# Optimization experiments

Hardware: AMD Instinct MI355X
Metric: run time of the kernel (lower is better)

## Reference

```python
import jax, jax.numpy as jnp
import numpy as np

N, D, F, E, TOP_K = 8192, 1024, 2048, 8, 2


def setup_inputs() -> dict:
    key = jax.random.key(0)
    ks = jax.random.split(key, 8)
    s = 0.02
    x = jax.random.normal(ks[0], (N, D), dtype=jnp.float32)
    Wr = jax.random.normal(ks[1], (D, E), dtype=jnp.float32) * s  # router
    br = jnp.zeros((E,), jnp.float32)
    W1 = jax.random.normal(ks[2], (E, D, F), dtype=jnp.float32) * s  # expert FFN in
    b1 = jnp.zeros((E, F), jnp.float32)
    W2 = jax.random.normal(ks[3], (E, F, D), dtype=jnp.float32) * s  # expert FFN out
    b2 = jnp.zeros((E, D), jnp. float32)
    return {"x": x, "Wr": Wr, "br": br, "W1": W1, "b1": b1, "W2": W2, "b2": b2}


def reference(x, Wr, br, W1, b1, W2, b2):
    # Router: per-token expert logits -> softmax probabilities -> top-k sampler.
    logits = x @ Wr + br                         # [N, E]
    probs = jax.nn.softmax(logits, axis=-1)      # [N, E]
    top_p, top_i = jax.lax.top_k(probs, TOP_K)   # [N, K]
    # Combine weights: prob mass only on the selected top-k experts per token.
    w = (jax.nn.one_hot(top_i, E, dtype=x.dtype) * top_p[..., None]).sum(axis=1)  # [N, E]
    # Per-expert gather-compute-scatter, expressed as masked full-batch expert FFN
    # (identical math: tokens not routed to expert e have weight 0).
    out = jnp.zeros((x.shape[0], W2.shape[-1]), dtype=x.dtype)
    for e in range(E):  # small fixed loop over structurally distinct experts
        h = jax.nn.gelu(x @ W1[e] + b1[e])       # [N, F]
        y = h @ W2[e] + b2[e]                    # [N, D]
        out = out + w[:, e:e + 1] * y            # weighted scatter-add combine
    return out
```

## Files before the change

kernel.cpp:

```cpp
#include <hip/hip_runtime.h>
#include <hip/hip_bf16.h>


#define N_TOK 8192
#define DIM   1024
#define FF    2048
#define NE    8

typedef unsigned short ushort_t;
typedef __bf16 bf16x8 __attribute__((ext_vector_type(8)));
typedef float  f32x4  __attribute__((ext_vector_type(4)));
typedef unsigned short u16x8 __attribute__((ext_vector_type(8)));

__device__ __forceinline__ ushort_t f2bf(float f) {
    union { float f; unsigned int u; } v; v.f = f;
    unsigned int r = (v.u + 0x7FFFu + ((v.u >> 16) & 1u)) >> 16;
    return (ushort_t)r;
}

__device__ __forceinline__ unsigned int pkbf2(float lo, float hi) {
    __hip_bfloat162 h = __float22bfloat162_rn(make_float2(lo, hi));
    return *reinterpret_cast<unsigned int*>(&h);
}

__device__ __forceinline__ void gload_lds16(const ushort_t* g, ushort_t* l) {
    __builtin_amdgcn_global_load_lds(
        (const __attribute__((address_space(1))) void*)g,
        (__attribute__((address_space(3))) void*)l,
        16, 0, 0);
}

__global__ __launch_bounds__(256) void convert_x_kernel(
    const float* __restrict__ x, ushort_t* __restrict__ xb)
{
    size_t i = ((size_t)blockIdx.x * 256 + threadIdx.x) * 8;
    float4 a = *reinterpret_cast<const float4*>(x + i);
    float4 b = *reinterpret_cast<const float4*>(x + i + 4);
    uint4 o;
    o.x = pkbf2(a.x, a.y); o.y = pkbf2(a.z, a.w);
    o.z = pkbf2(b.x, b.y); o.w = pkbf2(b.z, b.w);
    *reinterpret_cast<uint4*>(xb + i) = o;
}

__global__ __launch_bounds__(256) void transpose_conv_kernel(
    const float* __restrict__ in, ushort_t* __restrict__ out, int R, int C)
{
    __shared__ float tile[64][68];
    const int e = blockIdx.z;
    const float* I = in + (size_t)e * R * C;
    ushort_t*    O = out + (size_t)e * R * C;
    const int c0 = blockIdx.x * 64, r0 = blockIdx.y * 64;
    const int tid = threadIdx.x;
#pragma unroll
    for (int j = 0; j < 4; ++j) {
        int row = j * 16 + (tid >> 4);
        int col = (tid & 15) * 4;
        float4 v = *reinterpret_cast<const float4*>(&I[(size_t)(r0 + row) * C + c0 + col]);
        *reinterpret_cast<float4*>(&tile[row][col]) = v;
    }
    __syncthreads();
#pragma unroll
    for (int j = 0; j < 2; ++j) {
        int orow = j * 32 + (tid >> 3);
        int k0   = (tid & 7) * 8;
        uint4 o;
        o.x = pkbf2(tile[k0 + 0][orow], tile[k0 + 1][orow]);
        o.y = pkbf2(tile[k0 + 2][orow], tile[k0 + 3][orow]);
        o.z = pkbf2(tile[k0 + 4][orow], tile[k0 + 5][orow]);
        o.w = pkbf2(tile[k0 + 6][orow], tile[k0 + 7][orow]);
        *reinterpret_cast<uint4*>(&O[(size_t)(c0 + orow) * R + r0 + k0]) = o;
    }
}

__global__ __launch_bounds__(256) void router_kernel(
    const float* __restrict__ x, const float* __restrict__ Wr, const float* __restrict__ br,
    int* __restrict__ cnt, int* __restrict__ tok_list, float* __restrict__ w_list)
{
    __shared__ int   se0[64], se1[64];
    __shared__ float sw0[64], sw1[64];

    const int wid  = threadIdx.x >> 6;
    const int lane = threadIdx.x & 63;
    const int tblk = blockIdx.x * 64;

    for (int i = 0; i < 16; ++i) {
        const int li = wid * 16 + i;
        const int t  = tblk + li;
        const float* xr = x + (size_t)t * DIM;

        float acc[NE];
#pragma unroll
        for (int e = 0; e < NE; ++e) acc[e] = 0.f;
        for (int d = lane; d < DIM; d += 64) {
            float xv = xr[d];
            const float4* w4 = reinterpret_cast<const float4*>(Wr + (size_t)d * NE);
            float4 w0 = w4[0], w1 = w4[1];
            acc[0] += xv * w0.x; acc[1] += xv * w0.y; acc[2] += xv * w0.z; acc[3] += xv * w0.w;
            acc[4] += xv * w1.x; acc[5] += xv * w1.y; acc[6] += xv * w1.z; acc[7] += xv * w1.w;
        }
#pragma unroll
        for (int e = 0; e < NE; ++e) {
            for (int off = 32; off > 0; off >>= 1)
                acc[e] += __shfl_down(acc[e], off, 64);
        }
        if (lane == 0) {
            float l[NE];
#pragma unroll
            for (int e = 0; e < NE; ++e) l[e] = acc[e] + br[e];
            float mx = l[0];
#pragma unroll
            for (int e = 1; e < NE; ++e) mx = fmaxf(mx, l[e]);
            float p[NE], s = 0.f;
#pragma unroll
            for (int e = 0; e < NE; ++e) { p[e] = expf(l[e] - mx); s += p[e]; }
            float inv = 1.f / s;
            int e0 = 0;
#pragma unroll
            for (int e = 1; e < NE; ++e) if (l[e] > l[e0]) e0 = e;
            int e1 = (e0 == 0) ? 1 : 0;
#pragma unroll
            for (int e = 0; e < NE; ++e) if (e != e0 && l[e] > l[e1]) e1 = e;
            se0[li] = e0; sw0[li] = p[e0] * inv;
            se1[li] = e1; sw1[li] = p[e1] * inv;
        }
    }
    __syncthreads();

    if (threadIdx.x < 64) {
        const int t  = tblk + lane;
        const int e0 = se0[lane], e1 = se1[lane];
        const unsigned long long below = ((unsigned long long)1 << lane) - 1;
        int p0 = 0, p1 = 0;
#pragma unroll
        for (int e = 0; e < NE; ++e) {
            unsigned long long m0 = __ballot(e0 == e);
            unsigned long long m1 = __ballot(e1 == e);
            int c = __popcll(m0) + __popcll(m1);
            int b = 0;
            if (lane == e && c) b = atomicAdd(&cnt[e], c);
            b = __shfl(b, e, 64);
            if (e0 == e) p0 = b + __popcll(m0 & below);
            if (e1 == e) p1 = b + __popcll(m0) + __popcll(m1 & below);
        }
        tok_list[e0 * N_TOK + p0] = t;  w_list[e0 * N_TOK + p0] = sw0[lane];
        tok_list[e1 * N_TOK + p1] = t;  w_list[e1 * N_TOK + p1] = sw1[lane];
    }
}

__global__ void scan_kernel(const int* __restrict__ cnt, int* __restrict__ offs,
                            int* __restrict__ tile_e, int* __restrict__ tile_m0,
                            int* __restrict__ meta)
{
    if (threadIdx.x == 0 && blockIdx.x == 0) {
        int s = 0;
        for (int e = 0; e < NE; ++e) { offs[e] = s; s += cnt[e]; }
        offs[NE] = s;
        int nt = 0;
        for (int e = 0; e < NE; ++e)
            for (int m0 = 0; m0 < cnt[e]; m0 += 128) {
                tile_e[nt] = e; tile_m0[nt] = m0; ++nt;
            }
        meta[0] = nt;
    }
}

template <int MODE>
__global__ __launch_bounds__(512, 6) void moe_gemm_kernel(
    const ushort_t* __restrict__ A,
    const ushort_t* __restrict__ Bt,
    const float*    __restrict__ bias,
    const int*      __restrict__ cnt,
    const int*      __restrict__ offs,
    const int*      __restrict__ tok_list,
    const float*    __restrict__ w_list,
    const int*      __restrict__ tile_e,
    const int*      __restrict__ tile_m0,
    const int*      __restrict__ meta,
    ushort_t*       __restrict__ hout,
    float*          __restrict__ out)
{
    const int K    = (MODE == 0) ? 1024 : 2048;
    const int NCOL = (MODE == 0) ? 2048 : 1024;

    const int nmt = meta[0];
    const int L   = nmt << 4;

    const int xcd = blockIdx.x & 7;
    const int q = L >> 3, r = L & 7;
    const int cstart = (xcd < r) ? xcd * (q + 1) : r * (q + 1) + (xcd - r) * q;
    const int clen   = (xcd < r) ? q + 1 : q;

    __shared__ ushort_t smem[24576];
#define ASB(b) (smem + (b) * 4096)
#define BSB(b) (smem + 12288 + (b) * 4096)

    const int tid  = threadIdx.x;
    const int lane = tid & 63;
    const int wid  = tid >> 6;
    const int wr = (wid >> 2) * 64;
    const int wc = (wid & 3) * 32;
    const int la = lane & 15;
    const int kc = lane >> 4;

    for (int i = blockIdx.x >> 3; i < clen; i += 96) {
        const int tau = cstart + i;
        const int mt  = tau >> 4;
        int nb, kh;
        if (MODE == 0) { nb = tau & 15; kh = 0; }
        else           { kh = tau & 1;  nb = (tau >> 1) & 7; }
        const int e   = tile_e[mt];
        const int m0  = tile_m0[mt];
        const int cnt_e  = cnt[e];
        const int offs_e = offs[e];
        const int n0  = nb * 128;
        const int koff = kh << 10;

        __syncthreads();

        const int srow  = tid >> 2;
        const int chunk = (tid & 3) ^ ((srow >> 1) & 3);
        size_t asrc, bsrc;
        {
            int entry = m0 + srow;
            if (MODE == 0) {
                int tok = (entry < cnt_e) ? tok_list[e * N_TOK + entry] : 0;
                asrc = (size_t)tok * K + chunk * 8;
            } else {
                asrc = (size_t)(offs_e + entry) * K + koff + chunk * 8;
            }
            bsrc = ((size_t)e * NCOL + n0 + srow) * K + koff + chunk * 8;
        }

        f32x4 acc[4][2];
#pragma unroll
        for (int m = 0; m < 4; ++m)
#pragma unroll
            for (int n = 0; n < 2; ++n)
                acc[m][n] = (f32x4){0.f, 0.f, 0.f, 0.f};

        auto STAGE = [&](int t, int b) {
            int k0 = t * 32;
            gload_lds16(A  + asrc + k0, ASB(b) + tid * 8);
            gload_lds16(Bt + bsrc + k0, BSB(b) + tid * 8);
        };

        auto COMPUTE = [&](int b) {
            bf16x8 af[4], bfr[2];
#pragma unroll
            for (int m = 0; m < 4; ++m) {
                int rr = wr + m * 16 + la;
                af[m] = *reinterpret_cast<const bf16x8*>(ASB(b) + (rr * 4 + (kc ^ ((rr >> 1) & 3))) * 8);
            }
#pragma unroll
            for (int n = 0; n < 2; ++n) {
                int rr = wc + n * 16 + la;
                bfr[n] = *reinterpret_cast<const bf16x8*>(BSB(b) + (rr * 4 + (kc ^ ((rr >> 1) & 3))) * 8);
            }
            __builtin_amdgcn_s_setprio(1);
#pragma unroll
            for (int m = 0; m < 4; ++m)
#pragma unroll
                for (int n = 0; n < 2; ++n)
                    acc[m][n] = __builtin_amdgcn_mfma_f32_16x16x32_bf16(af[m], bfr[n], acc[m][n], 0, 0, 0);
            __builtin_amdgcn_s_setprio(0);
        };

        const int nk = 32;
        STAGE(0, 0);
        STAGE(1, 1);
        for (int t = 0; t < nk - 1; ++t) {
            asm volatile("s_waitcnt vmcnt(2)" ::: "memory");
            __builtin_amdgcn_s_barrier();
            if (t + 2 < nk) STAGE(t + 2, (t + 2) % 3);
            COMPUTE(t % 3);
        }
        asm volatile("s_waitcnt vmcnt(0)" ::: "memory");
        __builtin_amdgcn_s_barrier();
        COMPUTE((nk - 1) % 3);

        if (MODE == 0) {
            __syncthreads();
#pragma unroll
            for (int m = 0; m < 4; ++m) {
                int rbase = wr + m * 16 + (lane >> 4) * 4;
#pragma unroll
                for (int n = 0; n < 2; ++n) {
                    int ccol = wc + n * 16 + la;
                    float bi = bias[(size_t)e * NCOL + n0 + ccol];
#pragma unroll
                    for (int jj = 0; jj < 4; ++jj) {
                        float v = acc[m][n][jj] + bi;
                        float u = 0.7978845608028654f * (v + 0.044715f * v * v * v);
                        float t2 = __builtin_amdgcn_exp2f(2.8853900817779268f * u);
                        float g = v * (t2 / (t2 + 1.f));
                        smem[(rbase + jj) * 128 + ccol] = f2bf(g);
                    }
                }
            }
            __syncthreads();
#pragma unroll
            for (int j = 0; j < 4; ++j) {
                int c = tid + 512 * j;
                int row  = c >> 4;
                int col8 = (c & 15) * 8;
                int entry = m0 + row;
                if (entry < cnt_e) {
                    u16x8 v = *reinterpret_cast<const u16x8*>(&smem[row * 128 + col8]);
                    *reinterpret_cast<u16x8*>(&hout[(size_t)(offs_e + entry) * FF + n0 + col8]) = v;
                }
            }
        } else {
#pragma unroll
            for (int m = 0; m < 4; ++m) {
                int rbase = wr + m * 16 + (lane >> 4) * 4;
#pragma unroll
                for (int n = 0; n < 2; ++n) {
                    int gcol = n0 + wc + n * 16 + la;
                    float bi = (kh != 0) ? 0.f : bias[(size_t)e * NCOL + gcol];
#pragma unroll
                    for (int jj = 0; jj < 4; ++jj) {
                        int entry = m0 + rbase + jj;
                        if (entry < cnt_e) {
                            float v = acc[m][n][jj] + bi;
                            int tok  = tok_list[e * N_TOK + entry];
                            float w  = w_list  [e * N_TOK + entry];
                            atomicAdd(&out[(size_t)tok * DIM + gcol], w * v);
                        }
                    }
                }
            }
        }
    }
#undef ASB
#undef BSB
}

extern "C" void kernel_launch(void* const* d_in, const int* in_sizes, int n_in,
                              void* d_out, int out_size, void* d_ws, size_t ws_size,
                              hipStream_t stream)
{
    const float* x  = (const float*)d_in[0];
    const float* Wr = (const float*)d_in[1];
    const float* br = (const float*)d_in[2];
    const float* W1 = (const float*)d_in[3];
    const float* b1 = (const float*)d_in[4];
    const float* W2 = (const float*)d_in[5];
    const float* b2 = (const float*)d_in[6];
    float* out = (float*)d_out;

    char* ws = (char*)d_ws;
    size_t off = 0;
    auto alloc = [&](size_t bytes) -> void* {
        void* p = ws + off;
        off = (off + bytes + 255) & ~(size_t)255;
        return p;
    };
    ushort_t* w1t = (ushort_t*)alloc((size_t)NE * DIM * FF * 2);
    ushort_t* w2t = (ushort_t*)alloc((size_t)NE * DIM * FF * 2);
    ushort_t* xb  = (ushort_t*)alloc((size_t)N_TOK * DIM * 2);
    ushort_t* h   = (ushort_t*)alloc(((size_t)2 * N_TOK + 128) * FF * 2);
    int*      cnt = (int*)alloc(NE * sizeof(int));
    int*      offs= (int*)alloc((NE + 1) * sizeof(int));
    int*   tok_list = (int*)alloc((size_t)NE * N_TOK * sizeof(int));
    float* w_list   = (float*)alloc((size_t)NE * N_TOK * sizeof(float));
    int*   tile_e   = (int*)alloc(256 * sizeof(int));
    int*   tile_m0  = (int*)alloc(256 * sizeof(int));
    int*   meta     = (int*)alloc(16 * sizeof(int));
    (void)ws_size; (void)in_sizes; (void)n_in;

    hipMemsetAsync(out, 0, (size_t)out_size * sizeof(float), stream);
    hipMemsetAsync(cnt, 0, NE * sizeof(int), stream);

    convert_x_kernel<<<(N_TOK * DIM) / (8 * 256), 256, 0, stream>>>(x, xb);
    transpose_conv_kernel<<<dim3(FF / 64, DIM / 64, NE), 256, 0, stream>>>(W1, w1t, DIM, FF);
    transpose_conv_kernel<<<dim3(DIM / 64, FF / 64, NE), 256, 0, stream>>>(W2, w2t, FF, DIM);
    router_kernel<<<N_TOK / 64, 256, 0, stream>>>(x, Wr, br, cnt, tok_list, w_list);
    scan_kernel<<<1, 64, 0, stream>>>(cnt, offs, tile_e, tile_m0, meta);

    moe_gemm_kernel<0><<<768, 512, 0, stream>>>(
        xb, w1t, b1, cnt, offs, tok_list, w_list, tile_e, tile_m0, meta, h, nullptr);
    moe_gemm_kernel<1><<<768, 512, 0, stream>>>(
        h, w2t, b2, cnt, offs, tok_list, w_list, tile_e, tile_m0, meta, nullptr, out);
}
```

Baseline: 454.8 us.

## Pre-pack operands into MFMA fragment layout and load directly from global memory

Weights and the gathered token activations are now rearranged into a 16-row by 8-element fragment-packed bf16 layout, so each lane can read its MFMA operand with one 16-byte global load. The LDS staging pipeline and its barriers are removed in favour of register double-buffered direct loads. A new gather kernel builds an expert-sorted, padded activation buffer, which removes the per-tile token indirection in the first GEMM. Occupancy and grid size are lowered from 6 to 4 blocks per CU and from 768 to 512 blocks, and the GEMMs now rely on L2/cache hit rates instead of LDS reuse across waves.

```diff
diff --git a/kernel.cpp b/kernel.cpp
--- a/kernel.cpp
+++ b/kernel.cpp
@@ -6,6 +6,8 @@
 #define DIM   1024
 #define FF    2048
 #define NE    8
+#define ROWS_PAD 16512
+#define MAXTILE  1031
 
 typedef unsigned short ushort_t;
 typedef __bf16 bf16x8 __attribute__((ext_vector_type(8)));
@@ -21,55 +23,6 @@
 __device__ __forceinline__ unsigned int pkbf2(float lo, float hi) {
     __hip_bfloat162 h = __float22bfloat162_rn(make_float2(lo, hi));
     return *reinterpret_cast<unsigned int*>(&h);
-}
-
-__device__ __forceinline__ void gload_lds16(const ushort_t* g, ushort_t* l) {
-    __builtin_amdgcn_global_load_lds(
-        (const __attribute__((address_space(1))) void*)g,
-        (__attribute__((address_space(3))) void*)l,
-        16, 0, 0);
-}
-
-__global__ __launch_bounds__(256) void convert_x_kernel(
-    const float* __restrict__ x, ushort_t* __restrict__ xb)
-{
-    size_t i = ((size_t)blockIdx.x * 256 + threadIdx.x) * 8;
-    float4 a = *reinterpret_cast<const float4*>(x + i);
-    float4 b = *reinterpret_cast<const float4*>(x + i + 4);
-    uint4 o;
-    o.x = pkbf2(a.x, a.y); o.y = pkbf2(a.z, a.w);
-    o.z = pkbf2(b.x, b.y); o.w = pkbf2(b.z, b.w);
-    *reinterpret_cast<uint4*>(xb + i) = o;
-}
-
-__global__ __launch_bounds__(256) void transpose_conv_kernel(
-    const float* __restrict__ in, ushort_t* __restrict__ out, int R, int C)
-{
-    __shared__ float tile[64][68];
-    const int e = blockIdx.z;
-    const float* I = in + (size_t)e * R * C;
-    ushort_t*    O = out + (size_t)e * R * C;
-    const int c0 = blockIdx.x * 64, r0 = blockIdx.y * 64;
-    const int tid = threadIdx.x;
-#pragma unroll
-    for (int j = 0; j < 4; ++j) {
-        int row = j * 16 + (tid >> 4);
-        int col = (tid & 15) * 4;
-        float4 v = *reinterpret_cast<const float4*>(&I[(size_t)(r0 + row) * C + c0 + col]);
-        *reinterpret_cast<float4*>(&tile[row][col]) = v;
-    }
-    __syncthreads();
-#pragma unroll
-    for (int j = 0; j < 2; ++j) {
-        int orow = j * 32 + (tid >> 3);
-        int k0   = (tid & 7) * 8;
-        uint4 o;
-        o.x = pkbf2(tile[k0 + 0][orow], tile[k0 + 1][orow]);
-        o.y = pkbf2(tile[k0 + 2][orow], tile[k0 + 3][orow]);
-        o.z = pkbf2(tile[k0 + 4][orow], tile[k0 + 5][orow]);
-        o.w = pkbf2(tile[k0 + 6][orow], tile[k0 + 7][orow]);
-        *reinterpret_cast<uint4*>(&O[(size_t)(c0 + orow) * R + r0 + k0]) = o;
-    }
 }
 
 __global__ __launch_bounds__(256) void router_kernel(
@@ -147,14 +100,14 @@
     }
 }
 
-__global__ void scan_kernel(const int* __restrict__ cnt, int* __restrict__ offs,
+__global__ void scan_kernel(const int* __restrict__ cnt, int* __restrict__ aoffs,
                             int* __restrict__ tile_e, int* __restrict__ tile_m0,
                             int* __restrict__ meta)
 {
     if (threadIdx.x == 0 && blockIdx.x == 0) {
         int s = 0;
-        for (int e = 0; e < NE; ++e) { offs[e] = s; s += cnt[e]; }
-        offs[NE] = s;
+        for (int e = 0; e < NE; ++e) { aoffs[e] = s; s += (cnt[e] + 15) & ~15; }
+        aoffs[NE] = s;
         int nt = 0;
         for (int e = 0; e < NE; ++e)
             for (int m0 = 0; m0 < cnt[e]; m0 += 128) {
@@ -164,13 +117,74 @@
     }
 }
 
+__global__ __launch_bounds__(256) void gather_pack_kernel(
+    const float* __restrict__ x, const int* __restrict__ cnt,
+    const int* __restrict__ aoffs, const int* __restrict__ tok_list,
+    ushort_t* __restrict__ xpack)
+{
+    const int c   = blockIdx.x * 256 + threadIdx.x;
+    const int row = c >> 7;
+    const int d0  = (c & 127) << 3;
+    int e = 0;
+#pragma unroll
+    for (int k = 1; k < NE; ++k) e += (row >= aoffs[k]);
+    int entry = row - aoffs[e];
+    int ce = cnt[e];
+    if (entry >= ce) entry = (ce > 0) ? ce - 1 : 0;
+    const int tok = tok_list[e * N_TOK + entry] & (N_TOK - 1);
+    const float* src = x + ((size_t)tok << 10) + d0;
+    float4 a = *reinterpret_cast<const float4*>(src);
+    float4 b = *reinterpret_cast<const float4*>(src + 4);
+    u16x8 o;
+    o[0] = f2bf(a.x); o[1] = f2bf(a.y); o[2] = f2bf(a.z); o[3] = f2bf(a.w);
+    o[4] = f2bf(b.x); o[5] = f2bf(b.y); o[6] = f2bf(b.z); o[7] = f2bf(b.w);
+    size_t off = ((size_t)(row >> 4) * 128 + (d0 >> 3)) * 128 + (row & 15) * 8;
+    *reinterpret_cast<u16x8*>(xpack + off) = o;
+}
+
+__global__ __launch_bounds__(256) void transpose_pack_kernel(
+    const float* __restrict__ in, ushort_t* __restrict__ out, int R, int C)
+{
+    __shared__ float tile[64][68];
+    const int e = blockIdx.z;
+    const float* I = in + (size_t)e * R * C;
+    ushort_t*    O = out + (size_t)e * R * C;
+    const int c0 = blockIdx.x * 64, r0 = blockIdx.y * 64;
+    const int tid = threadIdx.x;
+#pragma unroll
+    for (int j = 0; j < 4; ++j) {
+        int row = j * 16 + (tid >> 4);
+        int col = (tid & 15) * 4;
+        float4 v = *reinterpret_cast<const float4*>(&I[(size_t)(r0 + row) * C + c0 + col]);
+        *reinterpret_cast<float4*>(&tile[row][col]) = v;
+    }
+    __syncthreads();
+    const int la  = tid & 15;
+    const int KC8 = R >> 3;
+#pragma unroll
+    for (int j = 0; j < 2; ++j) {
+        int u = (tid >> 4) + j * 16;
+        int ctile = u & 3, rchunk = u >> 2;
+        int col = ctile * 16 + la;
+        int rb  = rchunk * 8;
+        uint4 o;
+        o.x = pkbf2(tile[rb + 0][col], tile[rb + 1][col]);
+        o.y = pkbf2(tile[rb + 2][col], tile[rb + 3][col]);
+        o.z = pkbf2(tile[rb + 4][col], tile[rb + 5][col]);
+        o.w = pkbf2(tile[rb + 6][col], tile[rb + 7][col]);
+        int ctg = (c0 >> 4) + ctile;
+        int chk = (r0 >> 3) + rchunk;
+        *reinterpret_cast<uint4*>(&O[((size_t)ctg * KC8 + chk) * 128 + la * 8]) = o;
+    }
+}
+
 template <int MODE>
-__global__ __launch_bounds__(512, 6) void moe_gemm_kernel(
+__global__ __launch_bounds__(512, 4) void moe_gemm_kernel(
     const ushort_t* __restrict__ A,
     const ushort_t* __restrict__ Bt,
     const float*    __restrict__ bias,
     const int*      __restrict__ cnt,
-    const int*      __restrict__ offs,
+    const int*      __restrict__ aoffs,
     const int*      __restrict__ tok_list,
     const float*    __restrict__ w_list,
     const int*      __restrict__ tile_e,
@@ -179,8 +193,11 @@
     ushort_t*       __restrict__ hout,
     float*          __restrict__ out)
 {
-    const int K    = (MODE == 0) ? 1024 : 2048;
-    const int NCOL = (MODE == 0) ? 2048 : 1024;
+    const int K    = (MODE == 0) ? DIM : FF;
+    const int NCOL = (MODE == 0) ? FF : DIM;
+    const int KC8  = K >> 3;
+
+    __shared__ ushort_t smem[(MODE == 0) ? 128 * 136 : 16];
 
     const int nmt = meta[0];
     const int L   = nmt << 4;
@@ -189,10 +206,6 @@
     const int q = L >> 3, r = L & 7;
     const int cstart = (xcd < r) ? xcd * (q + 1) : r * (q + 1) + (xcd - r) * q;
     const int clen   = (xcd < r) ? q + 1 : q;
-
-    __shared__ ushort_t smem[24576];
-#define ASB(b) (smem + (b) * 4096)
-#define BSB(b) (smem + 12288 + (b) * 4096)
 
     const int tid  = threadIdx.x;
     const int lane = tid & 63;
@@ -202,7 +215,7 @@
     const int la = lane & 15;
     const int kc = lane >> 4;
 
-    for (int i = blockIdx.x >> 3; i < clen; i += 96) {
+    for (int i = blockIdx.x >> 3; i < clen; i += 64) {
         const int tau = cstart + i;
         const int mt  = tau >> 4;
         int nb, kh;
@@ -210,25 +223,22 @@
         else           { kh = tau & 1;  nb = (tau >> 1) & 7; }
         const int e   = tile_e[mt];
         const int m0  = tile_m0[mt];
-        const int cnt_e  = cnt[e];
-        const int offs_e = offs[e];
+        const int cnt_e = cnt[e];
+        const int am0   = aoffs[e] + m0;
         const int n0  = nb * 128;
-        const int koff = kh << 10;
-
-        __syncthreads();
-
-        const int srow  = tid >> 2;
-        const int chunk = (tid & 3) ^ ((srow >> 1) & 3);
-        size_t asrc, bsrc;
-        {
-            int entry = m0 + srow;
-            if (MODE == 0) {
-                int tok = (entry < cnt_e) ? tok_list[e * N_TOK + entry] : 0;
-                asrc = (size_t)tok * K + chunk * 8;
-            } else {
-                asrc = (size_t)(offs_e + entry) * K + koff + chunk * 8;
-            }
-            bsrc = ((size_t)e * NCOL + n0 + srow) * K + koff + chunk * 8;
+
+        unsigned int aB[4], bB[2];
+#pragma unroll
+        for (int m = 0; m < 4; ++m) {
+            int rt = ((am0 + wr) >> 4) + m;
+            if (rt > MAXTILE) rt = MAXTILE;
+            aB[m] = ((unsigned int)rt * KC8 + (MODE == 1 ? kh * 128 : 0) + kc) * 128 + la * 8;
+        }
+        const ushort_t* Be = Bt + (size_t)e * NCOL * K;
+#pragma unroll
+        for (int n = 0; n < 2; ++n) {
+            int ct = ((n0 + wc) >> 4) + n;
+            bB[n] = ((unsigned int)ct * KC8 + (MODE == 1 ? kh * 128 : 0) + kc) * 128 + la * 8;
         }
 
         f32x4 acc[4][2];
@@ -238,45 +248,35 @@
             for (int n = 0; n < 2; ++n)
                 acc[m][n] = (f32x4){0.f, 0.f, 0.f, 0.f};
 
-        auto STAGE = [&](int t, int b) {
-            int k0 = t * 32;
-            gload_lds16(A  + asrc + k0, ASB(b) + tid * 8);
-            gload_lds16(Bt + bsrc + k0, BSB(b) + tid * 8);
+        auto LOADF = [&](bf16x8* ar, bf16x8* br, int t) {
+            const unsigned int d = (unsigned int)t * 512u;
+#pragma unroll
+            for (int m = 0; m < 4; ++m)
+                ar[m] = *reinterpret_cast<const bf16x8*>(A + aB[m] + d);
+#pragma unroll
+            for (int n = 0; n < 2; ++n)
+                br[n] = *reinterpret_cast<const bf16x8*>(Be + bB[n] + d);
         };
-
-        auto COMPUTE = [&](int b) {
-            bf16x8 af[4], bfr[2];
-#pragma unroll
-            for (int m = 0; m < 4; ++m) {
-                int rr = wr + m * 16 + la;
-                af[m] = *reinterpret_cast<const bf16x8*>(ASB(b) + (rr * 4 + (kc ^ ((rr >> 1) & 3))) * 8);
-            }
-#pragma unroll
-            for (int n = 0; n < 2; ++n) {
-                int rr = wc + n * 16 + la;
-                bfr[n] = *reinterpret_cast<const bf16x8*>(BSB(b) + (rr * 4 + (kc ^ ((rr >> 1) & 3))) * 8);
-            }
+        auto MM = [&](const bf16x8* ar, const bf16x8* br) {
             __builtin_amdgcn_s_setprio(1);
 #pragma unroll
             for (int m = 0; m < 4; ++m)
 #pragma unroll
                 for (int n = 0; n < 2; ++n)
-                    acc[m][n] = __builtin_amdgcn_mfma_f32_16x16x32_bf16(af[m], bfr[n], acc[m][n], 0, 0, 0);
+                    acc[m][n] = __builtin_amdgcn_mfma_f32_16x16x32_bf16(
+                        ar[m], br[n], acc[m][n], 0, 0, 0);
             __builtin_amdgcn_s_setprio(0);
         };
 
+        bf16x8 a0[4], b0[2], a1[4], b1[2];
+        LOADF(a0, b0, 0);
         const int nk = 32;
-        STAGE(0, 0);
-        STAGE(1, 1);
-        for (int t = 0; t < nk - 1; ++t) {
-            asm volatile("s_waitcnt vmcnt(2)" ::: "memory");
-            __builtin_amdgcn_s_barrier();
-            if (t + 2 < nk) STAGE(t + 2, (t + 2) % 3);
-            COMPUTE(t % 3);
-        }
-        asm volatile("s_waitcnt vmcnt(0)" ::: "memory");
-        __builtin_amdgcn_s_barrier();
-        COMPUTE((nk - 1) % 3);
+        for (int t = 0; t < nk; t += 2) {
+            if (t + 1 < nk) LOADF(a1, b1, t + 1);
+            MM(a0, b0);
+            if (t + 2 < nk) LOADF(a0, b0, t + 2);
+            MM(a1, b1);
+        }
 
         if (MODE == 0) {
             __syncthreads();
@@ -293,7 +293,7 @@
                         float u = 0.7978845608028654f * (v + 0.044715f * v * v * v);
                         float t2 = __builtin_amdgcn_exp2f(2.8853900817779268f * u);
                         float g = v * (t2 / (t2 + 1.f));
-                        smem[(rbase + jj) * 128 + ccol] = f2bf(g);
+                        smem[(rbase + jj) * 136 + ccol] = f2bf(g);
                     }
                 }
             }
@@ -301,12 +301,16 @@
 #pragma unroll
             for (int j = 0; j < 4; ++j) {
                 int c = tid + 512 * j;
-                int row  = c >> 4;
-                int col8 = (c & 15) * 8;
+                int la2   = c & 15;
+                int colc  = (c >> 4) & 15;
+                int rowbk = c >> 8;
+                int row   = rowbk * 16 + la2;
                 int entry = m0 + row;
                 if (entry < cnt_e) {
-                    u16x8 v = *reinterpret_cast<const u16x8*>(&smem[row * 128 + col8]);
-                    *reinterpret_cast<u16x8*>(&hout[(size_t)(offs_e + entry) * FF + n0 + col8]) = v;
+                    int gr = am0 + row;
+                    u16x8 v = *reinterpret_cast<const u16x8*>(&smem[row * 136 + colc * 8]);
+                    size_t off = ((size_t)(gr >> 4) * 256 + ((n0 + colc * 8) >> 3)) * 128 + la2 * 8;
+                    *reinterpret_cast<u16x8*>(hout + off) = v;
                 }
             }
         } else {
@@ -331,8 +335,6 @@
             }
         }
     }
-#undef ASB
-#undef BSB
 }
 
 extern "C" void kernel_launch(void* const* d_in, const int* in_sizes, int n_in,
@@ -355,12 +357,12 @@
         off = (off + bytes + 255) & ~(size_t)255;
         return p;
     };
-    ushort_t* w1t = (ushort_t*)alloc((size_t)NE * DIM * FF * 2);
-    ushort_t* w2t = (ushort_t*)alloc((size_t)NE * DIM * FF * 2);
-    ushort_t* xb  = (ushort_t*)alloc((size_t)N_TOK * DIM * 2);
-    ushort_t* h   = (ushort_t*)alloc(((size_t)2 * N_TOK + 128) * FF * 2);
-    int*      cnt = (int*)alloc(NE * sizeof(int));
-    int*      offs= (int*)alloc((NE + 1) * sizeof(int));
+    ushort_t* w1t   = (ushort_t*)alloc((size_t)NE * DIM * FF * 2);
+    ushort_t* w2t   = (ushort_t*)alloc((size_t)NE * DIM * FF * 2);
+    ushort_t* xpack = (ushort_t*)alloc((size_t)ROWS_PAD * DIM * 2);
+    ushort_t* h     = (ushort_t*)alloc((size_t)ROWS_PAD * FF * 2);
+    int*      cnt   = (int*)alloc(NE * sizeof(int));
+    int*      aoffs = (int*)alloc((NE + 1) * sizeof(int));
     int*   tok_list = (int*)alloc((size_t)NE * N_TOK * sizeof(int));
     float* w_list   = (float*)alloc((size_t)NE * N_TOK * sizeof(float));
     int*   tile_e   = (int*)alloc(256 * sizeof(int));
@@ -371,14 +373,14 @@
     hipMemsetAsync(out, 0, (size_t)out_size * sizeof(float), stream);
     hipMemsetAsync(cnt, 0, NE * sizeof(int), stream);
 
-    convert_x_kernel<<<(N_TOK * DIM) / (8 * 256), 256, 0, stream>>>(x, xb);
-    transpose_conv_kernel<<<dim3(FF / 64, DIM / 64, NE), 256, 0, stream>>>(W1, w1t, DIM, FF);
-    transpose_conv_kernel<<<dim3(DIM / 64, FF / 64, NE), 256, 0, stream>>>(W2, w2t, FF, DIM);
+    transpose_pack_kernel<<<dim3(FF / 64, DIM / 64, NE), 256, 0, stream>>>(W1, w1t, DIM, FF);
+    transpose_pack_kernel<<<dim3(DIM / 64, FF / 64, NE), 256, 0, stream>>>(W2, w2t, FF, DIM);
     router_kernel<<<N_TOK / 64, 256, 0, stream>>>(x, Wr, br, cnt, tok_list, w_list);
-    scan_kernel<<<1, 64, 0, stream>>>(cnt, offs, tile_e, tile_m0, meta);
-
-    moe_gemm_kernel<0><<<768, 512, 0, stream>>>(
-        xb, w1t, b1, cnt, offs, tok_list, w_list, tile_e, tile_m0, meta, h, nullptr);
-    moe_gemm_kernel<1><<<768, 512, 0, stream>>>(
-        h, w2t, b2, cnt, offs, tok_list, w_list, tile_e, tile_m0, meta, nullptr, out);
-}
+    scan_kernel<<<1, 64, 0, stream>>>(cnt, aoffs, tile_e, tile_m0, meta);
+    gather_pack_kernel<<<(ROWS_PAD * 128) / 256, 256, 0, stream>>>(x, cnt, aoffs, tok_list, xpack);
+
+    moe_gemm_kernel<0><<<512, 512, 0, stream>>>(
+        xpack, w1t, b1, cnt, aoffs, tok_list, w_list, tile_e, tile_m0, meta, h, nullptr);
+    moe_gemm_kernel<1><<<512, 512, 0, stream>>>(
+        h, w2t, b2, cnt, aoffs, tok_list, w_list, tile_e, tile_m0, meta, nullptr, out);
+}
```

Result: slower. 584.8 us (+28.6%).
